# Kernel optimization log

Measured on AMD Instinct MI355X. Metric: run time of the kernel, lower is better.

Reference implementation:

```python
import jax, jax.numpy as jnp
from jax import lax
import numpy as np

NUM_EMBEDDINGS = 512
EMBEDDING_DIM = 64
COMMITMENT_COST = 0.25
SPARSITY_LEVEL = 8


def batch_omp(data, dictionary, max_nonzero):
    """Batch-OMP (Rubinstein et al.).
    data: [D, N], dictionary: [D, K] (columns unit-norm). Returns gamma [K, N].
    Runs a fixed max_nonzero greedy steps (the torch tolerance 1e-7 never
    triggers early exit on random data).
    """
    D, N = data.shape
    K = dictionary.shape[1]
    G = dictionary.T @ dictionary                 # [K, K] Gram matrix
    h_bar = (dictionary.T @ data).T               # [N, K] initial correlations
    h = h_bar
    mask = jnp.zeros((N, K), dtype=bool)          # selected-atom indicator
    rows = jnp.arange(N)
    L = jnp.ones((N, 1, 1), dtype=data.dtype)     # incremental Cholesky of G[I,I]
    I = None                                      # [N, k] selected indices
    x = jnp.zeros((N, K), dtype=data.dtype)
    for k in range(1, max_nonzero + 1):
        # greedy atom selection (masking already-chosen atoms)
        idx = jnp.argmax(jnp.abs(h * (~mask).astype(h.dtype)), axis=1)   # [N]
        mask = mask.at[rows, idx].set(True)
        if k > 1:
            g = G[I, idx[:, None]][..., None]                            # [N, k-1, 1]
            w = lax.linalg.triangular_solve(L, g, left_side=True, lower=True)
            w = jnp.swapaxes(w, 1, 2)                                    # [N, 1, k-1]
            w_corner = jnp.sqrt(1.0 - jnp.sum(w * w, axis=2, keepdims=True))
            top = jnp.concatenate([L, jnp.zeros((N, k - 1, 1), L.dtype)], axis=2)
            bot = jnp.concatenate([w, w_corner], axis=2)
            L = jnp.concatenate([top, bot], axis=1)                      # [N, k, k]
            I = jnp.concatenate([I, idx[:, None]], axis=1)
        else:
            I = idx[:, None]
        hb = jnp.take_along_axis(h_bar, I, axis=1)[..., None]            # [N, k, 1]
        # cholesky_solve: L L^T x = hb
        y = lax.linalg.triangular_solve(L, hb, left_side=True, lower=True)
        xs = lax.linalg.triangular_solve(L, y, left_side=True, lower=True,
                                         transpose_a=True)              # [N, k, 1]
        x = jnp.zeros((N, K), data.dtype).at[rows[:, None], I].set(xs[..., 0])
        beta = x @ G                                                     # x is zero off-support
        h = h_bar - beta
    return x.T                                                           # [K, N]


def setup_inputs() -> dict:
    key = jax.random.key(0)
    k1, k2 = jax.random.split(key)
    z_e = jax.random.normal(k1, (32, EMBEDDING_DIM, 32, 32), dtype=jnp.float32)
    dictionary = jax.random.normal(k2, (EMBEDDING_DIM, NUM_EMBEDDINGS), dtype=jnp.float32)
    beta = jnp.array([1.0 - COMMITMENT_COST], dtype=jnp.float32)  # nn.Parameter(1 - commitment_cost)
    return {"z_e": z_e, "dictionary": dictionary, "beta": beta}


def reference(z_e, dictionary, beta):
    # straight-through column normalization (torch does it via .data assignment)
    Dn_val = dictionary / jnp.linalg.norm(dictionary, axis=0)
    Dn = dictionary + lax.stop_gradient(Dn_val - dictionary)
    zp = jnp.transpose(z_e, (0, 2, 3, 1))                 # [B, H, W, C]
    ze_shape = zp.shape
    zf = zp.reshape(EMBEDDING_DIM, -1)                    # view(D, -1): [D, N]
    gamma = lax.stop_gradient(batch_omp(zf, Dn, SPARSITY_LEVEL))   # [K, N]; copied via .data in torch
    recon = Dn @ gamma                                    # [D, N]
    e_latent_loss = jnp.mean((lax.stop_gradient(recon) - zf) ** 2)
    q_loss = jnp.mean((recon - lax.stop_gradient(zf)) ** 2)
    loss = e_latent_loss * COMMITMENT_COST + beta[0] * q_loss
    recon_st = zf + lax.stop_gradient(recon - zf)         # straight-through
    sm = jax.nn.softmax(gamma, axis=0)
    perplexity = jnp.exp(-jnp.mean(jnp.sum(sm * jnp.log(sm + 1e-10), axis=0)))
    recon_out = jnp.transpose(recon_st.reshape(ze_shape), (0, 3, 1, 2))
    return loss, recon_out, lax.stop_gradient(zf), perplexity, gamma
```

## Files before the change

### kernel.cpp

```cpp
#include <hip/hip_runtime.h>
#include <math.h>

#define NCOL 32768
#define KAT  512
#define DIM  64
#define CPB  16

#define O_LOSS  0
#define O_RECON 1
#define O_ZF    2097153
#define O_PERP  4194305
#define O_GAMMA 4194306

#define WS_DN   0
#define WS_DNT  32768
#define WS_G    65536
#define WS_ACC  327680

__device__ __forceinline__ float wave_max_bcast_f32(float v) {
    int x = __float_as_int(v);
    int t;
    t = __builtin_amdgcn_update_dpp(x, x, 0x111, 0xf, 0xf, false);
    x = __float_as_int(fmaxf(__int_as_float(x), __int_as_float(t)));
    t = __builtin_amdgcn_update_dpp(x, x, 0x112, 0xf, 0xf, false);
    x = __float_as_int(fmaxf(__int_as_float(x), __int_as_float(t)));
    t = __builtin_amdgcn_update_dpp(x, x, 0x114, 0xf, 0xf, false);
    x = __float_as_int(fmaxf(__int_as_float(x), __int_as_float(t)));
    t = __builtin_amdgcn_update_dpp(x, x, 0x118, 0xf, 0xf, false);
    x = __float_as_int(fmaxf(__int_as_float(x), __int_as_float(t)));
    t = __builtin_amdgcn_update_dpp(x, x, 0x142, 0xa, 0xf, false);
    x = __float_as_int(fmaxf(__int_as_float(x), __int_as_float(t)));
    t = __builtin_amdgcn_update_dpp(x, x, 0x143, 0xc, 0xf, false);
    x = __float_as_int(fmaxf(__int_as_float(x), __int_as_float(t)));
    return __int_as_float(__builtin_amdgcn_readlane(x, 63));
}

__device__ __forceinline__ unsigned wave_min_bcast_u32(unsigned v) {
    int x = (int)v;
    int t;
    t = __builtin_amdgcn_update_dpp(x, x, 0x111, 0xf, 0xf, false);
    x = (int)min((unsigned)x, (unsigned)t);
    t = __builtin_amdgcn_update_dpp(x, x, 0x112, 0xf, 0xf, false);
    x = (int)min((unsigned)x, (unsigned)t);
    t = __builtin_amdgcn_update_dpp(x, x, 0x114, 0xf, 0xf, false);
    x = (int)min((unsigned)x, (unsigned)t);
    t = __builtin_amdgcn_update_dpp(x, x, 0x118, 0xf, 0xf, false);
    x = (int)min((unsigned)x, (unsigned)t);
    t = __builtin_amdgcn_update_dpp(x, x, 0x142, 0xa, 0xf, false);
    x = (int)min((unsigned)x, (unsigned)t);
    t = __builtin_amdgcn_update_dpp(x, x, 0x143, 0xc, 0xf, false);
    x = (int)min((unsigned)x, (unsigned)t);
    return (unsigned)__builtin_amdgcn_readlane(x, 63);
}

__device__ __forceinline__ float wave_sum_bcast_f32(float v) {
    int x = __float_as_int(v);
    int t;
    t = __builtin_amdgcn_update_dpp(x, x, 0x0B1, 0xf, 0xf, false);
    x = __float_as_int(__int_as_float(x) + __int_as_float(t));
    t = __builtin_amdgcn_update_dpp(x, x, 0x04E, 0xf, 0xf, false);
    x = __float_as_int(__int_as_float(x) + __int_as_float(t));
    t = __builtin_amdgcn_update_dpp(x, x, 0x141, 0xf, 0xf, false);
    x = __float_as_int(__int_as_float(x) + __int_as_float(t));
    t = __builtin_amdgcn_update_dpp(x, x, 0x140, 0xf, 0xf, false);
    x = __float_as_int(__int_as_float(x) + __int_as_float(t));
    t = __builtin_amdgcn_update_dpp(x, x, 0x142, 0xa, 0xf, false);
    x = __float_as_int(__int_as_float(x) + __int_as_float(t));
    t = __builtin_amdgcn_update_dpp(x, x, 0x143, 0xc, 0xf, false);
    x = __float_as_int(__int_as_float(x) + __int_as_float(t));
    return __int_as_float(__builtin_amdgcn_readlane(x, 63));
}

__device__ __forceinline__ float sum8_all_f32(float v) {
    int x = __float_as_int(v);
    int t;
    t = __builtin_amdgcn_update_dpp(x, x, 0x0B1, 0xf, 0xf, false);
    x = __float_as_int(__int_as_float(x) + __int_as_float(t));
    t = __builtin_amdgcn_update_dpp(x, x, 0x04E, 0xf, 0xf, false);
    x = __float_as_int(__int_as_float(x) + __int_as_float(t));
    t = __builtin_amdgcn_update_dpp(x, x, 0x141, 0xf, 0xf, false);
    x = __float_as_int(__int_as_float(x) + __int_as_float(t));
    return __int_as_float(x);
}

__global__ void prep_kernel(const float* __restrict__ dict, float* __restrict__ ws) {
    float* Dn  = ws + WS_DN;
    float* DnT = ws + WS_DNT;
    float* acc = ws + WS_ACC;
    int a = blockIdx.x * 64 + threadIdx.x;
    if (blockIdx.x == 0 && threadIdx.x < 2) acc[threadIdx.x] = 0.f;
    float s = 0.f;
    #pragma unroll
    for (int d = 0; d < DIM; ++d) { float v = dict[d*KAT + a]; s += v * v; }
    float nrm = sqrtf(s);
    #pragma unroll
    for (int d = 0; d < DIM; ++d) {
        float v = dict[d*KAT + a] / nrm;
        Dn[d*KAT + a]  = v;
        DnT[a*DIM + d] = v;
    }
}

__global__ void gram_kernel(const float* __restrict__ ws_in, float* __restrict__ ws) {
    const float* Dn = ws_in + WS_DN;
    float* G = ws + WS_G;
    int i = blockIdx.x, j = threadIdx.x;
    float s = 0.f;
    #pragma unroll
    for (int d = 0; d < DIM; ++d)
        s = fmaf(Dn[d*KAT + i], Dn[d*KAT + j], s);
    G[i*KAT + j] = s;
}

__global__ __launch_bounds__(256) void zg_kernel(const float* __restrict__ z_e,
                                                 float* __restrict__ out) {
    __shared__ float tile[64 * 33];
    int t = threadIdx.x;
    if (blockIdx.x < 1024) {
        int s = blockIdx.x;
        int b = s >> 5, h = s & 31;
        int srcbase = b * 65536 + h * 32;
        #pragma unroll
        for (int i = 0; i < 8; ++i) {
            int e = t + i * 256;
            int c = e >> 5, w = e & 31;
            tile[c * 33 + w] = z_e[srcbase + c * 1024 + w];
        }
        __syncthreads();
        int obase = O_ZF + s * 2048;
        #pragma unroll
        for (int i = 0; i < 8; ++i) {
            int e = t + i * 256;
            out[obase + e] = tile[(e & 63) * 33 + (e >> 6)];
        }
    } else {
        float2* g2 = (float2*)(out + O_GAMMA);
        int id = (blockIdx.x - 1024) * 256 + t;
        #pragma unroll
        for (int i = 0; i < 4; ++i)
            g2[id + i * 2097152] = make_float2(0.f, 0.f);
    }
}

__global__ __launch_bounds__(256, 4) void omp_kernel(const float* __restrict__ z_e,
                                                     const float* __restrict__ ws,
                                                     float* __restrict__ out,
                                                     float* __restrict__ wsw) {
    const float* Dn  = ws + WS_DN;
    const float* DnT = ws + WS_DNT;
    const float* G   = ws + WS_G;
    float* acc = wsw + WS_ACC;

    __shared__ __align__(16) float xcols[DIM * CPB];
    __shared__ float hbar[CPB * KAT];

    const int t = threadIdx.x;
    const int n_base = blockIdx.x * CPB;

    #pragma unroll
    for (int i = 0; i < 4; ++i) {
        int e = t + i * 256;
        int d = e >> 4, c = e & 15;
        int L = d * NCOL + n_base + c;
        int src = (L >> 16) * 65536 + (L & 63) * 1024 + (((L >> 11) & 31) << 5) + ((L >> 6) & 31);
        xcols[e] = z_e[src];
    }
    __syncthreads();

    {
        float a0[16], a1[16];
        #pragma unroll
        for (int i = 0; i < 16; ++i) { a0[i] = 0.f; a1[i] = 0.f; }
        const float4* xc4 = (const float4*)xcols;
        for (int d = 0; d < DIM; ++d) {
            float v0 = Dn[d * KAT + t];
            float v1 = Dn[d * KAT + 256 + t];
            #pragma unroll
            for (int q = 0; q < 4; ++q) {
                float4 xv = xc4[d * 4 + q];
                a0[q*4+0] = fmaf(v0, xv.x, a0[q*4+0]);
                a0[q*4+1] = fmaf(v0, xv.y, a0[q*4+1]);
                a0[q*4+2] = fmaf(v0, xv.z, a0[q*4+2]);
                a0[q*4+3] = fmaf(v0, xv.w, a0[q*4+3]);
                a1[q*4+0] = fmaf(v1, xv.x, a1[q*4+0]);
                a1[q*4+1] = fmaf(v1, xv.y, a1[q*4+1]);
                a1[q*4+2] = fmaf(v1, xv.z, a1[q*4+2]);
                a1[q*4+3] = fmaf(v1, xv.w, a1[q*4+3]);
            }
        }
        #pragma unroll
        for (int c = 0; c < 16; ++c) {
            hbar[c * KAT + t]       = a0[c];
            hbar[c * KAT + 256 + t] = a1[c];
        }
    }
    __syncthreads();

    const int wv = t >> 6, lane = t & 63;
    float wv_sq = 0.f, wv_S = 0.f;

    #pragma unroll 1
    for (int cc = 0; cc < 4; ++cc) {
        const int col = wv * 4 + cc;
        const int n = n_base + col;
        const float* hbcol = hbar + col * KAT;

        float h[8];
        #pragma unroll
        for (int r = 0; r < 8; ++r) h[r] = hbcol[(r << 6) + lane];

        unsigned msk = 0;
        float uv[56];
        float Lr[28];
        float invd[8], yv[8], xr[8];
        int Iv[8];

        #pragma unroll
        for (int k = 0; k < 8; ++k) {
            float bv = -1.f; int bi = 0; float hb = 0.f;
            #pragma unroll
            for (int r = 0; r < 8; ++r) {
                float av = ((msk >> r) & 1) ? -1.f : fabsf(h[r]);
                bool gt = av > bv;
                bv = gt ? av : bv;
                bi = gt ? ((r << 6) | lane) : bi;
                hb = gt ? h[r] : hb;
            }
            float maxv = wave_max_bcast_f32(bv);
            unsigned long long tie = __ballot(bv == maxv);
            int idx; float hwin;
            if (__popcll(tie) == 1) {
                int sl = __ffsll((unsigned long long)tie) - 1;
                idx  = __builtin_amdgcn_readlane(bi, sl);
                hwin = __int_as_float(__builtin_amdgcn_readlane(__float_as_int(hb), sl));
            } else {
                unsigned cand = (bv == maxv) ? (unsigned)bi : 0xffffffffu;
                idx = (int)wave_min_bcast_u32(cand);
                unsigned long long sm = __ballot((bv == maxv) && (bi == idx) && (hb < 0.f));
                hwin = (sm != 0ull) ? -maxv : maxv;
            }

            if ((idx & 63) == lane) msk |= 1u << (idx >> 6);
            Iv[k] = idx;

            const float* grow = G + idx * KAT;
            float gk[8];
            if (k < 7) {
                #pragma unroll
                for (int r = 0; r < 8; ++r) gk[r] = grow[(r << 6) + lane];
            }

            float Lk[7];
            if (k == 0) {
                invd[0] = 1.f;
            } else {
                float s2 = 0.f;
                #pragma unroll
                for (int i = 0; i < 7; ++i) if (i < k) {
                    float a = grow[Iv[i]];
                    #pragma unroll
                    for (int j = 0; j < 7; ++j) if (j < i) a = fmaf(-Lr[i*(i-1)/2 + j], Lk[j], a);
                    Lk[i] = a * invd[i];
                    s2 = fmaf(Lk[i], Lk[i], s2);
                }
                #pragma unroll
                for (int j = 0; j < 7; ++j) if (j < k) Lr[k*(k-1)/2 + j] = Lk[j];
                invd[k] = 1.f / sqrtf(1.f - s2);
            }
            yv[k] = hwin * invd[k];

            if (k < 7) {
                #pragma unroll
                for (int r = 0; r < 8; ++r) {
                    float a = gk[r];
                    #pragma unroll
                    for (int j = 0; j < 7; ++j) if (j < k) a = fmaf(-Lk[j], uv[j*8 + r], a);
                    a *= invd[k];
                    uv[k*8 + r] = a;
                    h[r] = fmaf(-yv[k], a, h[r]);
                }
            }
        }

        #pragma unroll
        for (int i = 7; i >= 0; --i) {
            float a = yv[i];
            #pragma unroll
            for (int j = 0; j < 8; ++j) if (j > i) a = fmaf(-Lr[j*(j-1)/2 + i], xr[j], a);
            xr[i] = a * invd[i];
        }

        #pragma unroll
        for (int j = 0; j < 8; ++j)
            if (lane == j) out[O_GAMMA + Iv[j] * NCOL + n] = xr[j];

        float rec = 0.f;
        #pragma unroll
        for (int j = 0; j < 8; ++j)
            rec = fmaf(xr[j], DnT[Iv[j] * DIM + lane], rec);
        int L = lane * NCOL + n;
        int perm = (L >> 16) * 65536 + (L & 63) * 1024 + (((L >> 11) & 31) << 5) + ((L >> 6) & 31);
        out[O_RECON + perm] = rec;

        float xd = xcols[lane * CPB + col];
        float diff = rec - xd;
        wv_sq += wave_sum_bcast_f32(diff * diff);

        {
            float m = 0.f;
            #pragma unroll
            for (int j = 0; j < 8; ++j) m = fmaxf(m, xr[j]);
            float xsel = 0.f;
            #pragma unroll
            for (int j = 0; j < 8; ++j) xsel = (lane == j) ? xr[j] : xsel;
            float e = (lane < 8) ? expf(xsel - m) : 0.f;
            float se = sum8_all_f32(e);
            float e0 = expf(-m);
            float Z = fmaf(504.f, e0, se);
            float invZ = 1.f / Z;
            float p = e * invZ;
            float tq = (lane < 8) ? p * logf(p + 1e-10f) : 0.f;
            tq = sum8_all_f32(tq);
            if (lane == 0) {
                float p0 = e0 * invZ;
                wv_S += tq + 504.f * p0 * logf(p0 + 1e-10f);
            }
        }
    }

    if (lane == 0) {
        atomicAdd(&acc[0], wv_sq);
        atomicAdd(&acc[1], wv_S);
    }
}

__global__ void fin_kernel(const float* __restrict__ ws, const float* __restrict__ beta,
                           float* __restrict__ out) {
    const float* acc = ws + WS_ACC;
    float mse = acc[0] / 2097152.f;
    out[O_LOSS] = mse * 0.25f + beta[0] * mse;
    out[O_PERP] = expf(-acc[1] / 32768.f);
}

extern "C" void kernel_launch(void* const* d_in, const int* in_sizes, int n_in,
                              void* d_out, int out_size, void* d_ws, size_t ws_size,
                              hipStream_t stream) {
    const float* z_e  = (const float*)d_in[0];
    const float* dict = (const float*)d_in[1];
    const float* beta = (const float*)d_in[2];
    float* out = (float*)d_out;
    float* ws  = (float*)d_ws;

    prep_kernel<<<8, 64, 0, stream>>>(dict, ws);
    gram_kernel<<<512, 512, 0, stream>>>(ws, ws);
    zg_kernel<<<9216, 256, 0, stream>>>(z_e, out);
    omp_kernel<<<2048, 256, 0, stream>>>(z_e, ws, out, ws);
    fin_kernel<<<1, 1, 0, stream>>>(ws, beta, out);
}
```

Baseline: 357.7 us.

## Fuse normalize, Gram and transpose into one prelaunch; zero gamma inside OMP kernel

Merges the dictionary normalization, Gram-matrix computation and z transpose into a single pre_kernel launch. The Gram blocks recompute the column norms directly from the raw dictionary, so they no longer depend on the normalization output. The separate pass that zeroed the large gamma output moves into the OMP kernel, where each block zeroes its own 16 columns before writing nonzeros. This removes two launches and a bulk memset pass, at the cost of redundant norm recomputation in the Gram blocks and strided zero stores inside OMP.

```diff
diff --git a/kernel.cpp b/kernel.cpp
--- a/kernel.cpp
+++ b/kernel.cpp
@@ -83,37 +83,10 @@
     return __int_as_float(x);
 }
 
-__global__ void prep_kernel(const float* __restrict__ dict, float* __restrict__ ws) {
-    float* Dn  = ws + WS_DN;
-    float* DnT = ws + WS_DNT;
-    float* acc = ws + WS_ACC;
-    int a = blockIdx.x * 64 + threadIdx.x;
-    if (blockIdx.x == 0 && threadIdx.x < 2) acc[threadIdx.x] = 0.f;
-    float s = 0.f;
-    #pragma unroll
-    for (int d = 0; d < DIM; ++d) { float v = dict[d*KAT + a]; s += v * v; }
-    float nrm = sqrtf(s);
-    #pragma unroll
-    for (int d = 0; d < DIM; ++d) {
-        float v = dict[d*KAT + a] / nrm;
-        Dn[d*KAT + a]  = v;
-        DnT[a*DIM + d] = v;
-    }
-}
-
-__global__ void gram_kernel(const float* __restrict__ ws_in, float* __restrict__ ws) {
-    const float* Dn = ws_in + WS_DN;
-    float* G = ws + WS_G;
-    int i = blockIdx.x, j = threadIdx.x;
-    float s = 0.f;
-    #pragma unroll
-    for (int d = 0; d < DIM; ++d)
-        s = fmaf(Dn[d*KAT + i], Dn[d*KAT + j], s);
-    G[i*KAT + j] = s;
-}
-
-__global__ __launch_bounds__(256) void zg_kernel(const float* __restrict__ z_e,
-                                                 float* __restrict__ out) {
+__global__ __launch_bounds__(256) void pre_kernel(const float* __restrict__ z_e,
+                                                  const float* __restrict__ dict,
+                                                  float* __restrict__ out,
+                                                  float* __restrict__ ws) {
     __shared__ float tile[64 * 33];
     int t = threadIdx.x;
     if (blockIdx.x < 1024) {
@@ -133,12 +106,42 @@
             int e = t + i * 256;
             out[obase + e] = tile[(e & 63) * 33 + (e >> 6)];
         }
+    } else if (blockIdx.x < 1026) {
+        float* Dn  = ws + WS_DN;
+        float* DnT = ws + WS_DNT;
+        float* acc = ws + WS_ACC;
+        int a = (blockIdx.x - 1024) * 256 + t;
+        if (blockIdx.x == 1024 && t < 2) acc[t] = 0.f;
+        float s = 0.f;
+        #pragma unroll
+        for (int d = 0; d < DIM; ++d) { float v = dict[d*KAT + a]; s += v * v; }
+        float nrm = sqrtf(s);
+        #pragma unroll
+        for (int d = 0; d < DIM; ++d) {
+            float v = dict[d*KAT + a] / nrm;
+            Dn[d*KAT + a]  = v;
+            DnT[a*DIM + d] = v;
+        }
     } else {
-        float2* g2 = (float2*)(out + O_GAMMA);
-        int id = (blockIdx.x - 1024) * 256 + t;
-        #pragma unroll
-        for (int i = 0; i < 4; ++i)
-            g2[id + i * 2097152] = make_float2(0.f, 0.f);
+        float* G = ws + WS_G;
+        int i = blockIdx.x - 1026;
+        float si = 0.f;
+        #pragma unroll
+        for (int d = 0; d < DIM; ++d) { float v = dict[d*KAT + i]; si += v * v; }
+        float ni = sqrtf(si);
+        #pragma unroll
+        for (int half = 0; half < 2; ++half) {
+            int j = t + half * 256;
+            float sj = 0.f;
+            #pragma unroll
+            for (int d = 0; d < DIM; ++d) { float v = dict[d*KAT + j]; sj += v * v; }
+            float nj = sqrtf(sj);
+            float dot = 0.f;
+            #pragma unroll
+            for (int d = 0; d < DIM; ++d)
+                dot = fmaf(dict[d*KAT + i] / ni, dict[d*KAT + j] / nj, dot);
+            G[i*KAT + j] = dot;
+        }
     }
 }
 
@@ -156,6 +159,16 @@
 
     const int t = threadIdx.x;
     const int n_base = blockIdx.x * CPB;
+
+    {
+        float2* gz = (float2*)(out + O_GAMMA + n_base);
+        int c2 = t & 7;
+        #pragma unroll
+        for (int i = 0; i < 16; ++i) {
+            int row = (t >> 3) + i * 32;
+            gz[row * (NCOL / 2) + c2] = make_float2(0.f, 0.f);
+        }
+    }
 
     #pragma unroll
     for (int i = 0; i < 4; ++i) {
@@ -351,9 +364,7 @@
     float* out = (float*)d_out;
     float* ws  = (float*)d_ws;
 
-    prep_kernel<<<8, 64, 0, stream>>>(dict, ws);
-    gram_kernel<<<512, 512, 0, stream>>>(ws, ws);
-    zg_kernel<<<9216, 256, 0, stream>>>(z_e, out);
+    pre_kernel<<<1538, 256, 0, stream>>>(z_e, dict, out, ws);
     omp_kernel<<<2048, 256, 0, stream>>>(z_e, ws, out, ws);
     fin_kernel<<<1, 1, 0, stream>>>(ws, beta, out);
 }
```

Measured after the change: 370.0 us. 1.03x slower.
